# Kernel tuning notes

Hardware: AMD Instinct MI355X
Metric: run time of the kernel (lower is better)

Reference implementation:

```python
import jax, jax.numpy as jnp
import numpy as np

B, C_IN, P, N = 4, 8, 12000, 64
C_PFN = 64          # PFN output channels (hardcoded in source)
H = W = 282         # BEV canvas size (hardcoded)
PILLAR = 0.16       # pillar size in meters
XMIN = YMIN = -22.0 # grid origin (x_edges/y_edges = arange(-22, 22, 0.16))
EPS = 1e-5          # BatchNorm eps (torch default)


def setup_inputs() -> dict:
    key = jax.random.key(0)
    ks = jax.random.split(key, 12)
    # coordinates/features uniform in the grid range so pillars land on the canvas
    sweep = jax.random.uniform(ks[0], (B, C_IN, P, N), jnp.float32, -22.0, 22.0)
    map_in = jax.random.uniform(ks[1], (B, C_IN, P, N), jnp.float32, -22.0, 22.0)
    s = 1.0 / np.sqrt(C_IN)
    w_sweep = jax.random.uniform(ks[2], (C_PFN, C_IN), jnp.float32, -s, s)
    b_sweep = jax.random.uniform(ks[3], (C_PFN,), jnp.float32, -s, s)
    gamma_sweep = 1.0 + 0.1 * jax.random.normal(ks[4], (C_PFN,), jnp.float32)
    beta_sweep = 0.1 * jax.random.normal(ks[5], (C_PFN,), jnp.float32)
    w_map = jax.random.uniform(ks[6], (C_PFN, C_IN), jnp.float32, -s, s)
    b_map = jax.random.uniform(ks[7], (C_PFN,), jnp.float32, -s, s)
    gamma_map = 1.0 + 0.1 * jax.random.normal(ks[8], (C_PFN,), jnp.float32)
    beta_map = 0.1 * jax.random.normal(ks[9], (C_PFN,), jnp.float32)
    sbb = 1.0 / np.sqrt(2 * C_PFN)
    w_bb = jax.random.uniform(ks[10], (C_PFN, 2 * C_PFN), jnp.float32, -sbb, sbb)
    b_bb = jax.random.uniform(ks[11], (C_PFN,), jnp.float32, -sbb, sbb)
    return {"sweep": sweep, "map_in": map_in,
            "w_sweep": w_sweep, "b_sweep": b_sweep,
            "gamma_sweep": gamma_sweep, "beta_sweep": beta_sweep,
            "w_map": w_map, "b_map": b_map,
            "gamma_map": gamma_map, "beta_map": beta_map,
            "w_bb": w_bb, "b_bb": b_bb}


def pfn(x, w, b, gamma, beta):
    # 1x1 conv: [B,8,P,N] -> [B,64,P,N]
    y = jnp.einsum('bcpn,oc->bopn', x, w) + b[None, :, None, None]
    # BatchNorm2d, training-mode batch stats over (B,P,N) per channel
    mean = y.mean(axis=(0, 2, 3), keepdims=True)
    var = y.var(axis=(0, 2, 3), keepdims=True)
    y = (y - mean) * jax.lax.rsqrt(var + EPS)
    y = y * gamma[None, :, None, None] + beta[None, :, None, None]
    y = jax.nn.relu(y)
    return y.max(axis=3)  # max over points -> [B,64,P]


def scatter_to_canvas(inp, feats):
    # inp: [B,8,P,N] (x,y coords at channels 0,1, point 0); feats: [B,64,P]
    x = inp[:, 0, :, 0]  # [B,P]
    y = inp[:, 1, :, 0]
    valid = x != 0  # pillar_list = nonzero(PFN_input[b,0,:,0])
    xg = jnp.clip(jnp.floor((x - XMIN) / PILLAR).astype(jnp.int32), 0, W - 1)
    yg = jnp.clip(jnp.floor((y - YMIN) / PILLAR).astype(jnp.int32), 0, H - 1)
    # route invalid pillars out of bounds so mode='drop' discards them
    xg = jnp.where(valid, xg, W)
    yg = jnp.where(valid, yg, H)
    bidx = jnp.broadcast_to(jnp.arange(B, dtype=jnp.int32)[:, None], (B, P))
    canvas = jnp.zeros((B, H, W, C_PFN), feats.dtype)
    canvas = canvas.at[bidx, yg, xg].set(jnp.swapaxes(feats, 1, 2), mode='drop')
    return jnp.transpose(canvas, (0, 3, 1, 2))  # [B,64,H,W]


def reference(sweep, map_in, w_sweep, b_sweep, gamma_sweep, beta_sweep,
              w_map, b_map, gamma_map, beta_map, w_bb, b_bb):
    sweep_feats = pfn(sweep, w_sweep, b_sweep, gamma_sweep, beta_sweep)
    map_feats = pfn(map_in, w_map, b_map, gamma_map, beta_map)
    sweep_canvas = scatter_to_canvas(sweep, sweep_feats)
    map_canvas = scatter_to_canvas(map_in, map_feats)
    cat = jnp.concatenate([sweep_canvas, map_canvas], axis=1)  # [B,128,H,W]
    # Backbone 1x1 conv (in-channels corrected to 128 to match the data)
    out = jnp.einsum('bchw,oc->bohw', cat, w_bb) + b_bb[None, :, None, None]
    return out
```

## Files before the change

### kernel.cpp

```cpp
#include <hip/hip_runtime.h>
#include <cfloat>
#include <math.h>

namespace {
constexpr int Bn = 4, Cin = 8, Pn = 12000, Nn = 64, Co = 64, Hh = 282, Ww = 282;
constexpr int NPIL  = Bn * Pn;
constexpr int NCELL = Hh * Ww;
constexpr int CHW   = Pn * Nn;
constexpr double CNTD = (double)Bn * Pn * Nn;
constexpr int K1B = 1024;
constexpr int WL_CAP = 48000;
constexpr int APPLY_B = (WL_CAP + 255) / 256;
constexpr int FILL_B = (Bn * Co * NCELL / 4) / 256;
constexpr int K5B = 2 * NPIL / 4;
constexpr int COMPACT_B = (Bn * NCELL + 255) / 256;

constexpr size_t PAR_OFF  = 0;
constexpr size_t HDR_OFF  = 5376;
constexpr size_t WLS_OFF  = 8192;
constexpr size_t PART_OFF = WLS_OFF;
constexpr size_t WLM_OFF  = WLS_OFF + (size_t)WL_CAP * 8;
constexpr size_t WIN_OFF  = WLM_OFF + (size_t)WL_CAP * 8;
constexpr size_t FEAT_OFF = WIN_OFF + (size_t)2 * Bn * NCELL * 4;
constexpr size_t WS_NEED  = FEAT_OFF + (size_t)2 * NPIL * 64 * 4;

typedef __attribute__((ext_vector_type(8))) float f32x8_t;
typedef __attribute__((ext_vector_type(2))) float f32x2_t;

__device__ __forceinline__ int cell_of(float xc, float yc) {
  int xg = (int)floorf((xc + 22.0f) * 6.25f);
  int yg = (int)floorf((yc + 22.0f) * 6.25f);
  xg = min(max(xg, 0), Ww - 1);
  yg = min(max(yg, 0), Hh - 1);
  return yg * Ww + xg;
}

__device__ __forceinline__ float firstlane(float v) {
  return __int_as_float(__builtin_amdgcn_readfirstlane(__float_as_int(v)));
}

__device__ __forceinline__ float dpp_xor1(float v) {
  return __int_as_float(__builtin_amdgcn_update_dpp(
      0, __float_as_int(v), 0xB1, 0xF, 0xF, true));
}
__device__ __forceinline__ float dpp_xor2(float v) {
  return __int_as_float(__builtin_amdgcn_update_dpp(
      0, __float_as_int(v), 0x4E, 0xF, 0xF, true));
}
}

__global__ void kdiag(float* __restrict__ out, float v) {
  if (threadIdx.x == 0 && blockIdx.x == 0) out[0] = v;
}

__global__ void k0_init(int* __restrict__ winners, int* __restrict__ hdr) {
  const int stride = gridDim.x * blockDim.x;
  const int t = blockIdx.x * blockDim.x + threadIdx.x;
  if (t < 8) hdr[t] = 0;
  for (int i = t; i < 2 * Bn * NCELL; i += stride) winners[i] = -1;
}

__global__ __launch_bounds__(256) void k_fillmom(
    const float* __restrict__ sweep, const float* __restrict__ map_in,
    const float* __restrict__ b_bb, float* __restrict__ out,
    float* __restrict__ partOut, int* __restrict__ winners)
{
  if (blockIdx.x < FILL_B) {
    const int idx = blockIdx.x * 256 + threadIdx.x;
    const int plane = idx / (NCELL / 4);
    const float v = b_bb[plane & 63];
    ((float4*)out)[idx] = make_float4(v, v, v, v);
    return;
  }
  __shared__ float red[4][44];
  const int bid  = blockIdx.x - FILL_B;
  const int lane = threadIdx.x & 63;
  const int wv   = threadIdx.x >> 6;
  const int bid2 = bid & (K1B - 1);
  const int inp  = bid / K1B;
  const float* x = inp ? map_in : sweep;
  int* win = winners + inp * Bn * NCELL;
  const int gw   = (bid2 * 256 + (int)threadIdx.x) >> 6;
  const int nw   = (K1B * 256) >> 6;
  constexpr int NG  = NPIL / 4;
  constexpr int GPB = Pn / 4;

  float sacc[8];
  float macc[36];
#pragma unroll
  for (int i = 0; i < 8; ++i) sacc[i] = 0.f;
#pragma unroll
  for (int i = 0; i < 36; ++i) macc[i] = 0.f;

  for (int g = gw; g < NG; g += nw) {
    const int b  = g / GPB;
    const int p0 = (g - b * GPB) * 4;
    const float4* xb4 =
        (const float4*)(x + (size_t)b * Cin * CHW + (size_t)p0 * Nn) + lane;
    float4 xv[Cin];
#pragma unroll
    for (int c = 0; c < Cin; ++c) xv[c] = xb4[(size_t)c * (CHW / 4)];
#pragma unroll
    for (int c = 0; c < Cin; ++c)
      sacc[c] += ((xv[c].x + xv[c].y) + (xv[c].z + xv[c].w));
    {
      int k = 0;
#pragma unroll
      for (int i = 0; i < 8; ++i)
#pragma unroll
        for (int j = i; j < 8; ++j) {
          float m = macc[k];
          m = fmaf(xv[i].x, xv[j].x, m);
          m = fmaf(xv[i].y, xv[j].y, m);
          m = fmaf(xv[i].z, xv[j].z, m);
          m = fmaf(xv[i].w, xv[j].w, m);
          macc[k] = m;
          ++k;
        }
    }
    if ((lane & 15) == 0) {
      const float xc = xv[0].x;
      if (xc != 0.0f) {
        const float yc = xv[1].x;
        atomicMax(&win[b * NCELL + cell_of(xc, yc)], p0 + (lane >> 4));
      }
    }
  }

#pragma unroll
  for (int k = 0; k < 44; ++k) {
    float v = (k < 8) ? sacc[k] : macc[k - 8];
#pragma unroll
    for (int off = 32; off > 0; off >>= 1) v += __shfl_down(v, off, 64);
    if (lane == 0) red[wv][k] = v;
  }
  __syncthreads();
  if (threadIdx.x < 44) {
    const float s = red[0][threadIdx.x] + red[1][threadIdx.x] +
                    red[2][threadIdx.x] + red[3][threadIdx.x];
    partOut[(size_t)bid2 * 88 + inp * 44 + threadIdx.x] = s;
  }
}

__global__ __launch_bounds__(512) void k1b2_params(
    const float* __restrict__ part,
    const float* __restrict__ w_s, const float* __restrict__ b_s,
    const float* __restrict__ g_s, const float* __restrict__ be_s,
    const float* __restrict__ w_m, const float* __restrict__ b_m,
    const float* __restrict__ g_m, const float* __restrict__ be_m,
    float* __restrict__ par)
{
  __shared__ double sd[88][4];
  __shared__ double smom[88];
  const int tid = threadIdx.x;
  if (tid < 352) {
    const int c = tid >> 2, q = tid & 3;
    double s = 0.0;
    for (int j = 0; j < K1B / 4; ++j)
      s += (double)part[(size_t)(q * (K1B / 4) + j) * 88 + c];
    sd[c][q] = s;
  }
  __syncthreads();
  if (tid < 88)
    smom[tid] = (sd[tid][0] + sd[tid][1]) + (sd[tid][2] + sd[tid][3]);
  __syncthreads();
  if (tid >= 128) return;
  const int inp = tid >> 6, o = tid & 63;
  const double* m = smom + inp * 44;
  const float* w    = (inp ? w_m : w_s) + o * Cin;
  const float bias  = (inp ? b_m : b_s)[o];
  const float gamma = (inp ? g_m : g_s)[o];
  const float beta  = (inp ? be_m : be_s)[o];
  double S[8];
#pragma unroll
  for (int c = 0; c < 8; ++c) S[c] = m[c] / CNTD;
  double mean = (double)bias;
#pragma unroll
  for (int c = 0; c < 8; ++c) mean += (double)w[c] * S[c];
  double var = 0.0;
  int k = 8;
#pragma unroll
  for (int i = 0; i < 8; ++i)
#pragma unroll
    for (int j = i; j < 8; ++j) {
      const double cov = m[k] / CNTD - S[i] * S[j];
      const double ww = (double)w[i] * (double)w[j];
      var += (i == j ? ww : 2.0 * ww) * cov;
      ++k;
    }
  const double a = (double)gamma / sqrt(var + 1e-5);
  float* pr = par + inp * 576;
#pragma unroll
  for (int c = 0; c < 8; ++c) pr[c * 64 + o] = (float)(a * (double)w[c]);
  pr[512 + o] = (float)((double)beta + a * ((double)bias - mean));
}

__global__ __launch_bounds__(256) void k5fc_feat(
    const float* __restrict__ sweep, const float* __restrict__ map_in,
    const float* __restrict__ par, const int* __restrict__ winners,
    int* __restrict__ hdr, int2* __restrict__ wlS, int2* __restrict__ wlM,
    float* __restrict__ feats)
{
  if (blockIdx.x >= K5B) {
    __shared__ int cS[4], cM[4];
    __shared__ int baseS, baseM;
    const int t = (blockIdx.x - K5B) * 256 + threadIdx.x;
    const int lane = threadIdx.x & 63;
    const int wvc  = threadIdx.x >> 6;
    int ps = -1, pm = -1, outbase = 0, b = 0;
    if (t < Bn * NCELL) {
      b = t / NCELL;
      const int hw = t - b * NCELL;
      outbase = b * Co * NCELL + hw;
      ps = winners[t];
      pm = winners[Bn * NCELL + t];
    }
    const unsigned long long ms = __ballot(ps >= 0);
    const unsigned long long mm = __ballot(pm >= 0);
    if (lane == 0) { cS[wvc] = __popcll(ms); cM[wvc] = __popcll(mm); }
    __syncthreads();
    if (threadIdx.x == 0) {
      const int c = cS[0] + cS[1] + cS[2] + cS[3];
      baseS = c ? atomicAdd(&hdr[1], c) : 0;
    } else if (threadIdx.x == 64) {
      const int c = cM[0] + cM[1] + cM[2] + cM[3];
      baseM = c ? atomicAdd(&hdr[2], c) : 0;
    }
    __syncthreads();
    const unsigned long long below = (1ull << lane) - 1ull;
    if (ps >= 0) {
      int off = baseS + __popcll(ms & below);
      for (int w2 = 0; w2 < wvc; ++w2) off += cS[w2];
      wlS[off] = make_int2(outbase, b * Pn + ps);
    }
    if (pm >= 0) {
      int off = baseM + __popcll(mm & below);
      for (int w2 = 0; w2 < wvc; ++w2) off += cM[w2];
      wlM[off] = make_int2(outbase, b * Pn + pm);
    }
    return;
  }

  const int lane = threadIdx.x & 63;
  const int wv   = __builtin_amdgcn_readfirstlane(threadIdx.x >> 6);
  int pp = blockIdx.x * 4 + wv;
  const int inp = (pp >= NPIL) ? 1 : 0;
  pp -= inp * NPIL;
  const float* x   = inp ? map_in : sweep;
  const float* awT = par + inp * 576;
  const float* zbp = awT + 512;
  const int*   win = winners + inp * Bn * NCELL;
  float*       ft  = feats + (size_t)inp * NPIL * 64;

  const int b = pp / Pn;
  const int p = pp - b * Pn;
  const size_t base = (size_t)b * Cin * CHW + (size_t)p * Nn;

  float xv[Cin];
#pragma unroll
  for (int c = 0; c < Cin; ++c) xv[c] = x[base + (size_t)c * CHW + lane];

  const float xc0 = firstlane(xv[0]);
  if (xc0 == 0.0f) return;
  const float yc0 = firstlane(xv[1]);
  const int cell = cell_of(xc0, yc0);
  if (win[b * NCELL + cell] != p) return;

  f32x2_t xd[Cin];
#pragma unroll
  for (int c = 0; c < Cin; ++c) xd[c] = (f32x2_t){xv[c], xv[c]};

  const int l0 = lane & 1, l1 = (lane >> 1) & 1, l2 = (lane >> 2) & 1;
  float res = 0.f;
#pragma unroll
  for (int g = 0; g < 8; ++g) {
    f32x8_t wr0, wr1, wr2, wr3, wr4, wr5, wr6, wr7, zb8;
    asm("s_load_dwordx8 %0, %9, 0x0\n\t"
        "s_load_dwordx8 %1, %9, 0x100\n\t"
        "s_load_dwordx8 %2, %9, 0x200\n\t"
        "s_load_dwordx8 %3, %9, 0x300\n\t"
        "s_load_dwordx8 %4, %9, 0x400\n\t"
        "s_load_dwordx8 %5, %9, 0x500\n\t"
        "s_load_dwordx8 %6, %9, 0x600\n\t"
        "s_load_dwordx8 %7, %9, 0x700\n\t"
        "s_load_dwordx8 %8, %10, 0x0\n\t"
        "s_waitcnt lgkmcnt(0)"
        : "=&s"(wr0), "=&s"(wr1), "=&s"(wr2), "=&s"(wr3), "=&s"(wr4),
          "=&s"(wr5), "=&s"(wr6), "=&s"(wr7), "=&s"(zb8)
        : "s"(awT + g * 8), "s"(zbp + g * 8));

    f32x2_t y0 = {zb8[0], zb8[1]};
    f32x2_t y1 = {zb8[2], zb8[3]};
    f32x2_t y2 = {zb8[4], zb8[5]};
    f32x2_t y3 = {zb8[6], zb8[7]};
#define CH(C, W)                                                              \
    {                                                                         \
      f32x2_t wpa = {W[0], W[1]}, wpb = {W[2], W[3]};                         \
      f32x2_t wpc = {W[4], W[5]}, wpd = {W[6], W[7]};                         \
      asm("v_pk_fma_f32 %0, %1, %2, %0" : "+v"(y0) : "s"(wpa), "v"(xd[C]));   \
      asm("v_pk_fma_f32 %0, %1, %2, %0" : "+v"(y1) : "s"(wpb), "v"(xd[C]));   \
      asm("v_pk_fma_f32 %0, %1, %2, %0" : "+v"(y2) : "s"(wpc), "v"(xd[C]));   \
      asm("v_pk_fma_f32 %0, %1, %2, %0" : "+v"(y3) : "s"(wpd), "v"(xd[C]));   \
    }
    CH(0, wr0) CH(1, wr1) CH(2, wr2) CH(3, wr3)
    CH(4, wr4) CH(5, wr5) CH(6, wr6) CH(7, wr7)
#undef CH
    float z[8] = {y0[0], y0[1], y1[0], y1[1], y2[0], y2[1], y3[0], y3[1]};

    float t0[4];
#pragma unroll
    for (int i = 0; i < 4; ++i) {
      const float send = l0 ? z[2 * i] : z[2 * i + 1];
      const float keep = l0 ? z[2 * i + 1] : z[2 * i];
      t0[i] = fmaxf(keep, dpp_xor1(send));
    }
    float t1[2];
#pragma unroll
    for (int i = 0; i < 2; ++i) {
      const float send = l1 ? t0[2 * i] : t0[2 * i + 1];
      const float keep = l1 ? t0[2 * i + 1] : t0[2 * i];
      t1[i] = fmaxf(keep, dpp_xor2(send));
    }
    {
      const float send = l2 ? t1[0] : t1[1];
      const float keep = l2 ? t1[1] : t1[0];
      float v = fmaxf(keep, __shfl_xor(send, 4, 64));
      v = fmaxf(v, __shfl_xor(v, 8, 64));
      v = fmaxf(v, __shfl_xor(v, 16, 64));
      v = fmaxf(v, __shfl_xor(v, 32, 64));
      if ((lane >> 3) == g) res = v;
    }
  }
  ft[(size_t)pp * 64 + lane] = fmaxf(res, 0.f);
}

template<int WHICH>
__global__ __launch_bounds__(256) void k_apply(
    const int* __restrict__ hdr, const int2* __restrict__ wl,
    const float* __restrict__ feats, const float* __restrict__ w_bb,
    const float* __restrict__ b_bb, float* __restrict__ out)
{
  __shared__ float4 wlds[Co * 16];
  __shared__ float bbb[Co];
  for (int i = threadIdx.x; i < Co * 16; i += 256)
    wlds[i] = ((const float4*)w_bb)[((i >> 4) << 5) + (WHICH ? 16 : 0) + (i & 15)];
  if (threadIdx.x < Co) bbb[threadIdx.x] = b_bb[threadIdx.x];
  __syncthreads();
  const int cnt = hdr[1 + WHICH];
  for (int i = blockIdx.x * blockDim.x + threadIdx.x; i < cnt;
       i += gridDim.x * blockDim.x) {
    const int2 e = wl[i];
    const float4* fp = (const float4*)(feats + (size_t)e.y * 64);
    float4 f[16];
#pragma unroll
    for (int k = 0; k < 16; ++k) f[k] = fp[k];
    float* op = out + e.x;
#pragma unroll 2
    for (int o = 0; o < Co; ++o) {
      float acc = WHICH ? op[(size_t)o * NCELL] : bbb[o];
      const float4* row = &wlds[o * 16];
#pragma unroll
      for (int k = 0; k < 16; ++k) {
        const float4 w4 = row[k];
        acc = fmaf(w4.x, f[k].x, acc); acc = fmaf(w4.y, f[k].y, acc);
        acc = fmaf(w4.z, f[k].z, acc); acc = fmaf(w4.w, f[k].w, acc);
      }
      op[(size_t)o * NCELL] = acc;
    }
  }
  if (WHICH == 1 && blockIdx.x == 0 && threadIdx.x == 0) {
    const int n_occ = hdr[1] + hdr[2];
    if (n_occ < 80000 || n_occ > 96000) out[0] = 1.0e7f + (float)n_occ;
  }
}

extern "C" void kernel_launch(void* const* d_in, const int* in_sizes, int n_in,
                              void* d_out, int out_size, void* d_ws, size_t ws_size,
                              hipStream_t stream)
{
  const float* sweep  = (const float*)d_in[0];
  const float* map_in = (const float*)d_in[1];
  const float* w_s  = (const float*)d_in[2];
  const float* b_s  = (const float*)d_in[3];
  const float* g_s  = (const float*)d_in[4];
  const float* be_s = (const float*)d_in[5];
  const float* w_m  = (const float*)d_in[6];
  const float* b_m  = (const float*)d_in[7];
  const float* g_m  = (const float*)d_in[8];
  const float* be_m = (const float*)d_in[9];
  const float* w_bb = (const float*)d_in[10];
  const float* b_bb = (const float*)d_in[11];
  float* out = (float*)d_out;

  const int exp_sz[12] = {24576000, 24576000, 512, 64, 64, 64, 512, 64, 64, 64, 8192, 64};
  int bad_idx = -1;
  if (n_in != 12) bad_idx = 11;
  else for (int i = 0; i < 12; ++i) if (in_sizes[i] != exp_sz[i]) { bad_idx = i; break; }
  if (bad_idx >= 0) {
    kdiag<<<1, 1, 0, stream>>>(out, 9.0e7f + 1.0e5f * (float)bad_idx);
    return;
  }
  if (ws_size < WS_NEED) {
    kdiag<<<1, 1, 0, stream>>>(out, 8.0e7f);
    return;
  }

  char* ws = (char*)d_ws;
  float*  par     = (float*)(ws + PAR_OFF);
  int*    hdr     = (int*)(ws + HDR_OFF);
  int*    winners = (int*)(ws + WIN_OFF);
  float*  feats   = (float*)(ws + FEAT_OFF);
  float*  part    = (float*)(ws + PART_OFF);
  int2*   wlS     = (int2*)(ws + WLS_OFF);
  int2*   wlM     = (int2*)(ws + WLM_OFF);

  k0_init<<<512, 256, 0, stream>>>(winners, hdr);
  k_fillmom<<<FILL_B + 2 * K1B, 256, 0, stream>>>(sweep, map_in, b_bb, out,
                                                  part, winners);
  k1b2_params<<<1, 512, 0, stream>>>(part, w_s, b_s, g_s, be_s,
                                     w_m, b_m, g_m, be_m, par);
  k5fc_feat<<<K5B + COMPACT_B, 256, 0, stream>>>(sweep, map_in, par, winners,
                                                 hdr, wlS, wlM, feats);
  k_apply<0><<<APPLY_B, 256, 0, stream>>>(hdr, wlS, feats, w_bb, b_bb, out);
  k_apply<1><<<APPLY_B, 256, 0, stream>>>(hdr, wlM, feats + (size_t)NPIL * 64,
                                          w_bb, b_bb, out);
}
```

Measured before the change: 312.3 us.

## Move winner compaction into single-block params kernel and reorder fill blocks

Winner-list compaction moves out of the feature kernel and into the single-block BN-parameter kernel, which now launches extra 512-thread blocks. The otherwise nearly idle params launch does that work, and the feature kernel shrinks to pure pillar work. The fill/moment kernel now issues the moment blocks first and the canvas-fill blocks after, so the reduction work starts earlier. The partial-sums buffer moves to the feature region so it no longer aliases the work lists written concurrently.

```diff
diff --git a/kernel.cpp b/kernel.cpp
--- a/kernel.cpp
+++ b/kernel.cpp
@@ -13,15 +13,15 @@
 constexpr int APPLY_B = (WL_CAP + 255) / 256;
 constexpr int FILL_B = (Bn * Co * NCELL / 4) / 256;
 constexpr int K5B = 2 * NPIL / 4;
-constexpr int COMPACT_B = (Bn * NCELL + 255) / 256;
+constexpr int COMPACT_B = (Bn * NCELL + 511) / 512;
 
 constexpr size_t PAR_OFF  = 0;
 constexpr size_t HDR_OFF  = 5376;
 constexpr size_t WLS_OFF  = 8192;
-constexpr size_t PART_OFF = WLS_OFF;
 constexpr size_t WLM_OFF  = WLS_OFF + (size_t)WL_CAP * 8;
 constexpr size_t WIN_OFF  = WLM_OFF + (size_t)WL_CAP * 8;
 constexpr size_t FEAT_OFF = WIN_OFF + (size_t)2 * Bn * NCELL * 4;
+constexpr size_t PART_OFF = FEAT_OFF;
 constexpr size_t WS_NEED  = FEAT_OFF + (size_t)2 * NPIL * 64 * 4;
 
 typedef __attribute__((ext_vector_type(8))) float f32x8_t;
@@ -65,15 +65,15 @@
     const float* __restrict__ b_bb, float* __restrict__ out,
     float* __restrict__ partOut, int* __restrict__ winners)
 {
-  if (blockIdx.x < FILL_B) {
-    const int idx = blockIdx.x * 256 + threadIdx.x;
+  if (blockIdx.x >= 2 * K1B) {
+    const int idx = (blockIdx.x - 2 * K1B) * 256 + threadIdx.x;
     const int plane = idx / (NCELL / 4);
     const float v = b_bb[plane & 63];
     ((float4*)out)[idx] = make_float4(v, v, v, v);
     return;
   }
   __shared__ float red[4][44];
-  const int bid  = blockIdx.x - FILL_B;
+  const int bid  = blockIdx.x;
   const int lane = threadIdx.x & 63;
   const int wv   = threadIdx.x >> 6;
   const int bid2 = bid & (K1B - 1);
@@ -142,105 +142,109 @@
   }
 }
 
-__global__ __launch_bounds__(512) void k1b2_params(
+__global__ __launch_bounds__(512) void k1b2c(
     const float* __restrict__ part,
     const float* __restrict__ w_s, const float* __restrict__ b_s,
     const float* __restrict__ g_s, const float* __restrict__ be_s,
     const float* __restrict__ w_m, const float* __restrict__ b_m,
     const float* __restrict__ g_m, const float* __restrict__ be_m,
-    float* __restrict__ par)
+    float* __restrict__ par, const int* __restrict__ winners,
+    int* __restrict__ hdr, int2* __restrict__ wlS, int2* __restrict__ wlM)
 {
-  __shared__ double sd[88][4];
-  __shared__ double smom[88];
-  const int tid = threadIdx.x;
-  if (tid < 352) {
-    const int c = tid >> 2, q = tid & 3;
-    double s = 0.0;
-    for (int j = 0; j < K1B / 4; ++j)
-      s += (double)part[(size_t)(q * (K1B / 4) + j) * 88 + c];
-    sd[c][q] = s;
-  }
+  if (blockIdx.x == 0) {
+    __shared__ double sd[88][4];
+    __shared__ double smom[88];
+    const int tid = threadIdx.x;
+    if (tid < 352) {
+      const int c = tid >> 2, q = tid & 3;
+      double s = 0.0;
+      for (int j = 0; j < K1B / 4; ++j)
+        s += (double)part[(size_t)(q * (K1B / 4) + j) * 88 + c];
+      sd[c][q] = s;
+    }
+    __syncthreads();
+    if (tid < 88)
+      smom[tid] = (sd[tid][0] + sd[tid][1]) + (sd[tid][2] + sd[tid][3]);
+    __syncthreads();
+    if (tid >= 128) return;
+    const int inp = tid >> 6, o = tid & 63;
+    const double* m = smom + inp * 44;
+    const float* w    = (inp ? w_m : w_s) + o * Cin;
+    const float bias  = (inp ? b_m : b_s)[o];
+    const float gamma = (inp ? g_m : g_s)[o];
+    const float beta  = (inp ? be_m : be_s)[o];
+    double S[8];
+#pragma unroll
+    for (int c = 0; c < 8; ++c) S[c] = m[c] / CNTD;
+    double mean = (double)bias;
+#pragma unroll
+    for (int c = 0; c < 8; ++c) mean += (double)w[c] * S[c];
+    double var = 0.0;
+    int k = 8;
+#pragma unroll
+    for (int i = 0; i < 8; ++i)
+#pragma unroll
+      for (int j = i; j < 8; ++j) {
+        const double cov = m[k] / CNTD - S[i] * S[j];
+        const double ww = (double)w[i] * (double)w[j];
+        var += (i == j ? ww : 2.0 * ww) * cov;
+        ++k;
+      }
+    const double a = (double)gamma / sqrt(var + 1e-5);
+    float* pr = par + inp * 576;
+#pragma unroll
+    for (int c = 0; c < 8; ++c) pr[c * 64 + o] = (float)(a * (double)w[c]);
+    pr[512 + o] = (float)((double)beta + a * ((double)bias - mean));
+    return;
+  }
+
+  __shared__ int cS[8], cM[8];
+  __shared__ int baseS, baseM;
+  const int t = (int)(blockIdx.x - 1) * 512 + (int)threadIdx.x;
+  const int lane = threadIdx.x & 63;
+  const int wvc  = threadIdx.x >> 6;
+  int ps = -1, pm = -1, outbase = 0, b = 0;
+  if (t < Bn * NCELL) {
+    b = t / NCELL;
+    const int hw = t - b * NCELL;
+    outbase = b * Co * NCELL + hw;
+    ps = winners[t];
+    pm = winners[Bn * NCELL + t];
+  }
+  const unsigned long long ms = __ballot(ps >= 0);
+  const unsigned long long mm = __ballot(pm >= 0);
+  if (lane == 0) { cS[wvc] = __popcll(ms); cM[wvc] = __popcll(mm); }
   __syncthreads();
-  if (tid < 88)
-    smom[tid] = (sd[tid][0] + sd[tid][1]) + (sd[tid][2] + sd[tid][3]);
+  if (threadIdx.x == 0) {
+    int c = 0;
+#pragma unroll
+    for (int i = 0; i < 8; ++i) c += cS[i];
+    baseS = c ? atomicAdd(&hdr[1], c) : 0;
+  } else if (threadIdx.x == 64) {
+    int c = 0;
+#pragma unroll
+    for (int i = 0; i < 8; ++i) c += cM[i];
+    baseM = c ? atomicAdd(&hdr[2], c) : 0;
+  }
   __syncthreads();
-  if (tid >= 128) return;
-  const int inp = tid >> 6, o = tid & 63;
-  const double* m = smom + inp * 44;
-  const float* w    = (inp ? w_m : w_s) + o * Cin;
-  const float bias  = (inp ? b_m : b_s)[o];
-  const float gamma = (inp ? g_m : g_s)[o];
-  const float beta  = (inp ? be_m : be_s)[o];
-  double S[8];
-#pragma unroll
-  for (int c = 0; c < 8; ++c) S[c] = m[c] / CNTD;
-  double mean = (double)bias;
-#pragma unroll
-  for (int c = 0; c < 8; ++c) mean += (double)w[c] * S[c];
-  double var = 0.0;
-  int k = 8;
-#pragma unroll
-  for (int i = 0; i < 8; ++i)
-#pragma unroll
-    for (int j = i; j < 8; ++j) {
-      const double cov = m[k] / CNTD - S[i] * S[j];
-      const double ww = (double)w[i] * (double)w[j];
-      var += (i == j ? ww : 2.0 * ww) * cov;
-      ++k;
-    }
-  const double a = (double)gamma / sqrt(var + 1e-5);
-  float* pr = par + inp * 576;
-#pragma unroll
-  for (int c = 0; c < 8; ++c) pr[c * 64 + o] = (float)(a * (double)w[c]);
-  pr[512 + o] = (float)((double)beta + a * ((double)bias - mean));
-}
-
-__global__ __launch_bounds__(256) void k5fc_feat(
+  const unsigned long long below = (1ull << lane) - 1ull;
+  if (ps >= 0) {
+    int off = baseS + __popcll(ms & below);
+    for (int w2 = 0; w2 < wvc; ++w2) off += cS[w2];
+    wlS[off] = make_int2(outbase, b * Pn + ps);
+  }
+  if (pm >= 0) {
+    int off = baseM + __popcll(mm & below);
+    for (int w2 = 0; w2 < wvc; ++w2) off += cM[w2];
+    wlM[off] = make_int2(outbase, b * Pn + pm);
+  }
+}
+
+__global__ __launch_bounds__(256) void k5f_feat(
     const float* __restrict__ sweep, const float* __restrict__ map_in,
     const float* __restrict__ par, const int* __restrict__ winners,
-    int* __restrict__ hdr, int2* __restrict__ wlS, int2* __restrict__ wlM,
     float* __restrict__ feats)
 {
-  if (blockIdx.x >= K5B) {
-    __shared__ int cS[4], cM[4];
-    __shared__ int baseS, baseM;
-    const int t = (blockIdx.x - K5B) * 256 + threadIdx.x;
-    const int lane = threadIdx.x & 63;
-    const int wvc  = threadIdx.x >> 6;
-    int ps = -1, pm = -1, outbase = 0, b = 0;
-    if (t < Bn * NCELL) {
-      b = t / NCELL;
-      const int hw = t - b * NCELL;
-      outbase = b * Co * NCELL + hw;
-      ps = winners[t];
-      pm = winners[Bn * NCELL + t];
-    }
-    const unsigned long long ms = __ballot(ps >= 0);
-    const unsigned long long mm = __ballot(pm >= 0);
-    if (lane == 0) { cS[wvc] = __popcll(ms); cM[wvc] = __popcll(mm); }
-    __syncthreads();
-    if (threadIdx.x == 0) {
-      const int c = cS[0] + cS[1] + cS[2] + cS[3];
-      baseS = c ? atomicAdd(&hdr[1], c) : 0;
-    } else if (threadIdx.x == 64) {
-      const int c = cM[0] + cM[1] + cM[2] + cM[3];
-      baseM = c ? atomicAdd(&hdr[2], c) : 0;
-    }
-    __syncthreads();
-    const unsigned long long below = (1ull << lane) - 1ull;
-    if (ps >= 0) {
-      int off = baseS + __popcll(ms & below);
-      for (int w2 = 0; w2 < wvc; ++w2) off += cS[w2];
-      wlS[off] = make_int2(outbase, b * Pn + ps);
-    }
-    if (pm >= 0) {
-      int off = baseM + __popcll(mm & below);
-      for (int w2 = 0; w2 < wvc; ++w2) off += cM[w2];
-      wlM[off] = make_int2(outbase, b * Pn + pm);
-    }
-    return;
-  }
-
   const int lane = threadIdx.x & 63;
   const int wv   = __builtin_amdgcn_readfirstlane(threadIdx.x >> 6);
   int pp = blockIdx.x * 4 + wv;
@@ -415,12 +419,12 @@
   int2*   wlM     = (int2*)(ws + WLM_OFF);
 
   k0_init<<<512, 256, 0, stream>>>(winners, hdr);
-  k_fillmom<<<FILL_B + 2 * K1B, 256, 0, stream>>>(sweep, map_in, b_bb, out,
+  k_fillmom<<<2 * K1B + FILL_B, 256, 0, stream>>>(sweep, map_in, b_bb, out,
                                                   part, winners);
-  k1b2_params<<<1, 512, 0, stream>>>(part, w_s, b_s, g_s, be_s,
-                                     w_m, b_m, g_m, be_m, par);
-  k5fc_feat<<<K5B + COMPACT_B, 256, 0, stream>>>(sweep, map_in, par, winners,
-                                                 hdr, wlS, wlM, feats);
+  k1b2c<<<1 + COMPACT_B, 512, 0, stream>>>(part, w_s, b_s, g_s, be_s,
+                                           w_m, b_m, g_m, be_m, par,
+                                           winners, hdr, wlS, wlM);
+  k5f_feat<<<K5B, 256, 0, stream>>>(sweep, map_in, par, winners, feats);
   k_apply<0><<<APPLY_B, 256, 0, stream>>>(hdr, wlS, feats, w_bb, b_bb, out);
   k_apply<1><<<APPLY_B, 256, 0, stream>>>(hdr, wlM, feats + (size_t)NPIL * 64,
                                           w_bb, b_bb, out);
```

New measurement: 294.1 us. 5.8% less time.
